# Kernel optimization log

Hardware: AMD Instinct MI355X
Metric: run time of the kernel (lower is better)

## Reference

```python
import jax, jax.numpy as jnp
import numpy as np

D_INV = 1024
N_HEADS = 8
D_HEAD = D_INV // N_HEADS
NEG_INF = -1e9  # masked-out logit value (adj_to_attn_mask)


def setup_inputs() -> dict:
    key = jax.random.key(0)
    ks = jax.random.split(key, 7)
    B, Nq, Nkv = 2, 2048, 2048
    v_inv = jax.random.normal(ks[0], (B, Nkv, D_INV), dtype=jnp.float32)
    messages = jax.random.normal(ks[1], (B, Nq, Nkv, N_HEADS), dtype=jnp.float32)
    adj_matrix = jax.random.randint(ks[2], (B, Nq, Nkv), 0, 2, dtype=jnp.int32)
    scale = 1.0 / np.sqrt(D_INV)
    in_w = jax.random.normal(ks[3], (D_INV, D_INV), dtype=jnp.float32) * scale
    in_b = jax.random.normal(ks[4], (D_INV,), dtype=jnp.float32) * 0.01
    out_w = jax.random.normal(ks[5], (D_INV, D_INV), dtype=jnp.float32) * scale
    out_b = jax.random.normal(ks[6], (D_INV,), dtype=jnp.float32) * 0.01
    return {"v_inv": v_inv, "messages": messages, "adj_matrix": adj_matrix,
            "in_w": in_w, "in_b": in_b, "out_w": out_w, "out_b": out_b}


def reference(v_inv, messages, adj_matrix, in_w, in_b, out_w, out_b):
    B, Nq, Nkv, H = messages.shape
    d_head = v_inv.shape[-1] // H
    # in_proj + split heads: [B, Nkv, H, d_head]
    proj = jnp.einsum('bkd,ed->bke', v_inv, in_w) + in_b
    head_feats = proj.reshape(B, Nkv, H, d_head)
    # adjacency -> additive mask, broadcast over heads
    attn_mask = jnp.where(adj_matrix != 0, 0.0, NEG_INF).astype(messages.dtype)
    logits = messages + attn_mask[..., None]            # [B, Nq, Nkv, H]
    attn = jax.nn.softmax(logits, axis=2)               # softmax over N_kv
    # per-head aggregation: [B, Nq, H, d_head]
    attn_out = jnp.einsum('bqkh,bkhd->bqhd', attn, head_feats)
    # L2-norm weight rescale over N_kv: [B, Nq, H]
    weights = jnp.sqrt(jnp.sum(attn * attn, axis=2))
    attn_out = attn_out * weights[..., None]
    attn_out = attn_out.reshape(B, Nq, H * d_head)
    return jnp.einsum('bqe,de->bqd', attn_out, out_w) + out_b
```

## Files before the change

kernel.cpp:

```cpp
#include <hip/hip_runtime.h>
#include <hip/hip_bf16.h>

typedef float f32x4 __attribute__((ext_vector_type(4)));
typedef __bf16 bf16x8 __attribute__((ext_vector_type(8)));

__device__ __forceinline__ unsigned short f2bf(float f) {
    union { float f; unsigned int u; } v; v.f = f;
    unsigned int u = v.u;
    unsigned int r = (u + 0x7fffu + ((u >> 16) & 1u)) >> 16;
    return (unsigned short)r;
}
__device__ __forceinline__ float bf2f(unsigned short u) {
    union { unsigned int u; float f; } v; v.u = ((unsigned int)u) << 16;
    return v.f;
}

__device__ __forceinline__ void block_sync_lgkm() {
    __asm__ __volatile__("" ::: "memory");
    __builtin_amdgcn_s_waitcnt(0xC07F);
    __builtin_amdgcn_s_barrier();
    __asm__ __volatile__("" ::: "memory");
}

__global__ __launch_bounds__(256) void k_cvt(const float* __restrict__ in,
                                             unsigned short* __restrict__ out, int n4) {
    int i = blockIdx.x * 256 + threadIdx.x;
    if (i >= n4) return;
    float4 v = ((const float4*)in)[i];
    ushort4 o;
    o.x = f2bf(v.x); o.y = f2bf(v.y); o.z = f2bf(v.z); o.w = f2bf(v.w);
    ((ushort4*)out)[i] = o;
}

__global__ __launch_bounds__(256, 4) void k_gemm_in(const unsigned short* __restrict__ A,
                                                    const unsigned short* __restrict__ B,
                                                    const float* __restrict__ bias,
                                                    unsigned short* __restrict__ Vfrag) {
    __shared__ __align__(16) unsigned short As[2][128 * 32];
    __shared__ __align__(16) unsigned short Bs[2][64 * 32];
    const int t = threadIdx.x;
    const int wv = t >> 6, lane = t & 63, mr = lane & 15, quad = lane >> 4;
    const int wi = wv >> 1, wj = wv & 1;
    const int m0 = blockIdx.y * 128, n0 = blockIdx.x * 64;

    f32x4 acc[4][2] = {};
    const int ra0 = t >> 2, ra1 = (t >> 2) + 64, rb = t >> 2;
    const int koff = (t & 3) * 8;

    uint4 pa0 = *(const uint4*)(A + (size_t)(m0 + ra0) * 1024 + koff);
    uint4 pa1 = *(const uint4*)(A + (size_t)(m0 + ra1) * 1024 + koff);
    uint4 pb  = *(const uint4*)(B + (size_t)(n0 + rb)  * 1024 + koff);

    for (int kb = 0; kb < 32; kb++) {
        unsigned short* as = As[kb & 1];
        unsigned short* bs = Bs[kb & 1];
        *(uint4*)&as[ra0 * 32 + koff] = pa0;
        *(uint4*)&as[ra1 * 32 + koff] = pa1;
        *(uint4*)&bs[rb  * 32 + koff] = pb;
        if (kb < 31) {
            int kk = (kb + 1) * 32 + koff;
            pa0 = *(const uint4*)(A + (size_t)(m0 + ra0) * 1024 + kk);
            pa1 = *(const uint4*)(A + (size_t)(m0 + ra1) * 1024 + kk);
            pb  = *(const uint4*)(B + (size_t)(n0 + rb)  * 1024 + kk);
        }
        block_sync_lgkm();
        bf16x8 af[4], bf[2];
        #pragma unroll
        for (int i = 0; i < 4; i++)
            af[i] = *(const bf16x8*)&as[(wi * 64 + i * 16 + mr) * 32 + quad * 8];
        #pragma unroll
        for (int j = 0; j < 2; j++)
            bf[j] = *(const bf16x8*)&bs[(wj * 32 + j * 16 + mr) * 32 + quad * 8];
        #pragma unroll
        for (int i = 0; i < 4; i++)
        #pragma unroll
        for (int j = 0; j < 2; j++)
            acc[i][j] = __builtin_amdgcn_mfma_f32_16x16x32_bf16(af[i], bf[j], acc[i][j], 0, 0, 0);
    }
    #pragma unroll
    for (int i = 0; i < 4; i++)
    #pragma unroll
    for (int j = 0; j < 2; j++) {
        int col = n0 + wj * 32 + j * 16 + mr;
        int row0 = m0 + wi * 64 + i * 16 + quad * 4;
        float be = bias[col];
        int h = col >> 7, d = col & 127;
        int bb = row0 >> 11, k = row0 & 2047;
        size_t idx8 = ((((size_t)(bb * 8 + h) * 64 + (k >> 5)) * 8 + (d >> 4)) * 64
                       + ((k >> 3) & 3) * 16 + (d & 15));
        int j0 = (quad & 1) * 4;
        ushort4 pk;
        pk.x = f2bf(acc[i][j][0] + be);
        pk.y = f2bf(acc[i][j][1] + be);
        pk.z = f2bf(acc[i][j][2] + be);
        pk.w = f2bf(acc[i][j][3] + be);
        *(ushort4*)(Vfrag + idx8 * 8 + j0) = pk;
    }
}

__global__ __launch_bounds__(256, 4) void k_gemm_out(const unsigned short* __restrict__ W,
                                                     const unsigned short* __restrict__ AOS,
                                                     const float* __restrict__ bias,
                                                     float* __restrict__ out) {
    __shared__ __align__(16) unsigned short As[2][128 * 32];
    __shared__ __align__(16) unsigned short Bs[2][64 * 32];
    const int t = threadIdx.x;
    const int wv = t >> 6, lane = t & 63, mr = lane & 15, quad = lane >> 4;
    const int wi = wv >> 1, wj = wv & 1;
    const int e0 = blockIdx.y * 128, r0 = blockIdx.x * 64;

    f32x4 acc[4][2] = {};
    const int ra0 = t >> 2, ra1 = (t >> 2) + 64, rb = t >> 2;
    const int koff = (t & 3) * 8;

    uint4 pa0 = *(const uint4*)(W   + (size_t)(e0 + ra0) * 1024 + koff);
    uint4 pa1 = *(const uint4*)(W   + (size_t)(e0 + ra1) * 1024 + koff);
    uint4 pb  = *(const uint4*)(AOS + (size_t)(r0 + rb)  * 1024 + koff);

    for (int kb = 0; kb < 32; kb++) {
        unsigned short* as = As[kb & 1];
        unsigned short* bs = Bs[kb & 1];
        *(uint4*)&as[ra0 * 32 + koff] = pa0;
        *(uint4*)&as[ra1 * 32 + koff] = pa1;
        *(uint4*)&bs[rb  * 32 + koff] = pb;
        if (kb < 31) {
            int kk = (kb + 1) * 32 + koff;
            pa0 = *(const uint4*)(W   + (size_t)(e0 + ra0) * 1024 + kk);
            pa1 = *(const uint4*)(W   + (size_t)(e0 + ra1) * 1024 + kk);
            pb  = *(const uint4*)(AOS + (size_t)(r0 + rb)  * 1024 + kk);
        }
        block_sync_lgkm();
        bf16x8 af[4], bf[2];
        #pragma unroll
        for (int i = 0; i < 4; i++)
            af[i] = *(const bf16x8*)&as[(wi * 64 + i * 16 + mr) * 32 + quad * 8];
        #pragma unroll
        for (int j = 0; j < 2; j++)
            bf[j] = *(const bf16x8*)&bs[(wj * 32 + j * 16 + mr) * 32 + quad * 8];
        #pragma unroll
        for (int i = 0; i < 4; i++)
        #pragma unroll
        for (int j = 0; j < 2; j++)
            acc[i][j] = __builtin_amdgcn_mfma_f32_16x16x32_bf16(af[i], bf[j], acc[i][j], 0, 0, 0);
    }
    #pragma unroll
    for (int i = 0; i < 4; i++)
    #pragma unroll
    for (int j = 0; j < 2; j++) {
        int r_ = r0 + wj * 32 + j * 16 + mr;
        int e_ = e0 + wi * 64 + i * 16 + quad * 4;
        float4 bv = *(const float4*)&bias[e_];
        float4 o;
        o.x = acc[i][j][0] + bv.x;
        o.y = acc[i][j][1] + bv.y;
        o.z = acc[i][j][2] + bv.z;
        o.w = acc[i][j][3] + bv.w;
        *(float4*)&out[(size_t)r_ * 1024 + e_] = o;
    }
}

__global__ __launch_bounds__(512, 2) void k_attn(const float* __restrict__ msg,
                                                 const int* __restrict__ adj,
                                                 const unsigned short* __restrict__ Vfrag,
                                                 unsigned short* __restrict__ AOS) {
    __shared__ __align__(16) unsigned short lds_p[2][4096];
    __shared__ float lds_w[8][16];
    __shared__ __align__(16) unsigned short lds_t[16 * 1032];

    const int t = threadIdx.x;
    const int wg = (int)blockIdx.x;
    const int swz = (wg & 7) * 32 + (wg >> 3);
    const int b = swz >> 7;
    const int q0 = (swz & 127) * 16;

    const int wv = t >> 6, lane = t & 63, mr = lane & 15, quad = lane >> 4;
    const int kl = lane >> 1;
    const int h0 = (lane & 1) * 4;
    const int lm0 = wv;

    const float* msg_base = msg + (size_t)(b * 2048 + q0) * 2048 * 8;
    const int* adj_base = adj + (size_t)(b * 2048 + q0) * 2048;
    const unsigned short* vf_base =
        Vfrag + (((size_t)(b * 8 + wv) * 64 * 8) * 64 + lane) * 8;

    const float* mp0 = msg_base + (size_t)lm0 * 16384 + kl * 8 + h0;
    const float* mp1 = mp0 + 8 * 16384;
    const int* ap0 = adj_base + lm0 * 2048 + kl;
    const int* ap1 = ap0 + 8 * 2048;

    float4 m0r = *(const float4*)mp0;
    float4 m1r = *(const float4*)mp1;
    int a0r = ap0[0], a1r = ap1[0];
    bf16x8 vfR[8];
    #pragma unroll
    for (int nc = 0; nc < 8; nc++) vfR[nc] = *(const bf16x8*)(vf_base + nc * 512);

    float laccs[2][4] = {}, saccs[2][4] = {};
    f32x4 acc[8] = {};

    const int sr = wv * 4 + quad;
    const int afrag_off = (sr * 16 + (mr ^ (sr & 15))) * 8;

    for (int kb = 0; kb < 64; kb++) {
        unsigned short* pbuf = lds_p[kb & 1];
        float px[2][4] = {{m0r.x, m0r.y, m0r.z, m0r.w}, {m1r.x, m1r.y, m1r.z, m1r.w}};
        float bl[2];
        bl[0] = a0r ? 0.f : -1e30f;
        bl[1] = a1r ? 0.f : -1e30f;
        #pragma unroll
        for (int qi = 0; qi < 2; qi++) {
            #pragma unroll
            for (int hj = 0; hj < 4; hj++) {
                float pe = __expf(px[qi][hj] + bl[qi]);
                laccs[qi][hj] += pe;
                saccs[qi][hj] = fmaf(pe, pe, saccs[qi][hj]);
                int s = (h0 + hj) * 4 + (kl >> 3);
                int m = lm0 + qi * 8;
                pbuf[(s * 16 + (m ^ (s & 15))) * 8 + (kl & 7)] = f2bf(pe);
            }
        }
        if (kb < 63) {
            m0r = *(const float4*)(mp0 + (kb + 1) * 256);
            m1r = *(const float4*)(mp1 + (kb + 1) * 256);
            a0r = ap0[(kb + 1) * 32];
            a1r = ap1[(kb + 1) * 32];
        }
        block_sync_lgkm();
        bf16x8 afrag = *(const bf16x8*)&pbuf[afrag_off];
        #pragma unroll
        for (int nc = 0; nc < 8; nc++)
            acc[nc] = __builtin_amdgcn_mfma_f32_16x16x32_bf16(afrag, vfR[nc], acc[nc], 0, 0, 0);
        if (kb < 63) {
            const unsigned short* vp = vf_base + (size_t)(kb + 1) * 4096;
            #pragma unroll
            for (int nc = 0; nc < 8; nc++) vfR[nc] = *(const bf16x8*)(vp + nc * 512);
        }
    }

    #pragma unroll
    for (int qi = 0; qi < 2; qi++)
    #pragma unroll
    for (int hj = 0; hj < 4; hj++) {
        float l = laccs[qi][hj], s = saccs[qi][hj];
        #pragma unroll
        for (int mdist = 2; mdist <= 32; mdist <<= 1) {
            l += __shfl_xor(l, mdist, 64);
            s += __shfl_xor(s, mdist, 64);
        }
        laccs[qi][hj] = l; saccs[qi][hj] = s;
    }
    if (lane < 2) {
        #pragma unroll
        for (int qi = 0; qi < 2; qi++)
        #pragma unroll
        for (int hj = 0; hj < 4; hj++) {
            float l = laccs[qi][hj];
            lds_w[lane * 4 + hj][wv + qi * 8] = __fsqrt_rn(saccs[qi][hj]) / (l * l);
        }
    }
    block_sync_lgkm();

    float4 wq = *(const float4*)&lds_w[wv][quad * 4];
    float wqa[4] = {wq.x, wq.y, wq.z, wq.w};
    #pragma unroll
    for (int nc = 0; nc < 8; nc++) {
        int e = wv * 128 + nc * 16 + mr;
        #pragma unroll
        for (int j = 0; j < 4; j++)
            lds_t[(quad * 4 + j) * 1032 + e] = f2bf(acc[nc][j] * wqa[j]);
    }
    block_sync_lgkm();
    #pragma unroll
    for (int p = 0; p < 4; p++) {
        int le = (p * 512 + t) * 8;
        int q = le >> 10, e = le & 1023;
        uint4 v = *(const uint4*)&lds_t[q * 1032 + e];
        *(uint4*)(AOS + (size_t)(b * 2048 + q0 + q) * 1024 + e) = v;
    }
}

extern "C" void kernel_launch(void* const* d_in, const int* in_sizes, int n_in,
                              void* d_out, int out_size, void* d_ws, size_t ws_size,
                              hipStream_t stream) {
    const float* v_inv    = (const float*)d_in[0];
    const float* messages = (const float*)d_in[1];
    const int*   adjm     = (const int*)d_in[2];
    const float* in_w     = (const float*)d_in[3];
    const float* in_b     = (const float*)d_in[4];
    const float* out_w    = (const float*)d_in[5];
    const float* out_b    = (const float*)d_in[6];
    float* out = (float*)d_out;

    char* ws = (char*)d_ws;
    unsigned short* vinv_bf = (unsigned short*)(ws);
    unsigned short* inw_bf  = (unsigned short*)(ws + (size_t)(8  << 20));
    unsigned short* outw_bf = (unsigned short*)(ws + (size_t)(10 << 20));
    unsigned short* Vfrag   = (unsigned short*)(ws + (size_t)(12 << 20));
    unsigned short* AOS     = (unsigned short*)(ws + (size_t)(20 << 20));

    hipLaunchKernelGGL(k_cvt, dim3(4096), dim3(256), 0, stream, v_inv, vinv_bf, 4194304 / 4);
    hipLaunchKernelGGL(k_cvt, dim3(1024), dim3(256), 0, stream, in_w, inw_bf, 1048576 / 4);
    hipLaunchKernelGGL(k_cvt, dim3(1024), dim3(256), 0, stream, out_w, outw_bf, 1048576 / 4);
    hipLaunchKernelGGL(k_gemm_in, dim3(16, 32), dim3(256), 0, stream, vinv_bf, inw_bf, in_b, Vfrag);
    hipLaunchKernelGGL(k_attn, dim3(256), dim3(512), 0, stream, messages, adjm, Vfrag, AOS);
    hipLaunchKernelGGL(k_gemm_out, dim3(64, 8), dim3(256), 0, stream, outw_bf, AOS, out_b, out);
}
```

Before: 460.9 us.

## Rework projection GEMMs with direct-to-LDS loads, triple buffering, larger tiles

Both projection GEMMs move to 128x128 tiles with a K step of 64. Tiles are staged straight into LDS with global_load_lds and a three-deep buffer ring managed by explicit vmcnt waits, replacing the register-staged double buffer. The three fp32-to-bf16 conversion launches are merged into one kernel to cut launch overhead. The larger LDS footprint (96 KB) and accumulator count lower occupancy, and the grids shrink to 256 blocks, which may underfill the device.

```diff
diff --git a/kernel.cpp b/kernel.cpp
--- a/kernel.cpp
+++ b/kernel.cpp
@@ -22,66 +22,92 @@
     __asm__ __volatile__("" ::: "memory");
 }
 
-__global__ __launch_bounds__(256) void k_cvt(const float* __restrict__ in,
-                                             unsigned short* __restrict__ out, int n4) {
-    int i = blockIdx.x * 256 + threadIdx.x;
-    if (i >= n4) return;
-    float4 v = ((const float4*)in)[i];
+__global__ __launch_bounds__(256) void k_cvt3(const float* __restrict__ a, unsigned short* __restrict__ oa,
+                                              const float* __restrict__ b, unsigned short* __restrict__ ob,
+                                              const float* __restrict__ c, unsigned short* __restrict__ oc) {
+    int id = blockIdx.x;
+    const float* src; unsigned short* dst; int i;
+    if (id < 4096)      { src = a; dst = oa; i = id * 256 + threadIdx.x; }
+    else if (id < 5120) { src = b; dst = ob; i = (id - 4096) * 256 + threadIdx.x; }
+    else                { src = c; dst = oc; i = (id - 5120) * 256 + threadIdx.x; }
+    float4 v = ((const float4*)src)[i];
     ushort4 o;
     o.x = f2bf(v.x); o.y = f2bf(v.y); o.z = f2bf(v.z); o.w = f2bf(v.w);
-    ((ushort4*)out)[i] = o;
-}
-
-__global__ __launch_bounds__(256, 4) void k_gemm_in(const unsigned short* __restrict__ A,
+    ((ushort4*)dst)[i] = o;
+}
+
+__device__ __forceinline__ void stage_tile(const unsigned short* __restrict__ g, int row0,
+                                           int ks, unsigned short* lds, int t) {
+    const int wv = t >> 6, lane = t & 63;
+    const unsigned short* gsrc = g + (size_t)(row0 + (lane >> 3)) * 1024 + ks * 64 + (lane & 7) * 8;
+    unsigned short* ldst = lds + wv * 512;
+    #pragma unroll
+    for (int i = 0; i < 4; i++) {
+        __builtin_amdgcn_global_load_lds(
+            (const __attribute__((address_space(1))) unsigned int*)(gsrc + (size_t)(i * 32 + wv * 8) * 1024),
+            (__attribute__((address_space(3))) unsigned int*)(ldst + i * 2048), 16, 0, 0);
+    }
+}
+
+__global__ __launch_bounds__(256, 2) void k_gemm_in(const unsigned short* __restrict__ A,
                                                     const unsigned short* __restrict__ B,
                                                     const float* __restrict__ bias,
                                                     unsigned short* __restrict__ Vfrag) {
-    __shared__ __align__(16) unsigned short As[2][128 * 32];
-    __shared__ __align__(16) unsigned short Bs[2][64 * 32];
+    __shared__ __align__(16) unsigned short As[3][128 * 64];
+    __shared__ __align__(16) unsigned short Bs[3][128 * 64];
     const int t = threadIdx.x;
     const int wv = t >> 6, lane = t & 63, mr = lane & 15, quad = lane >> 4;
     const int wi = wv >> 1, wj = wv & 1;
-    const int m0 = blockIdx.y * 128, n0 = blockIdx.x * 64;
-
-    f32x4 acc[4][2] = {};
-    const int ra0 = t >> 2, ra1 = (t >> 2) + 64, rb = t >> 2;
-    const int koff = (t & 3) * 8;
-
-    uint4 pa0 = *(const uint4*)(A + (size_t)(m0 + ra0) * 1024 + koff);
-    uint4 pa1 = *(const uint4*)(A + (size_t)(m0 + ra1) * 1024 + koff);
-    uint4 pb  = *(const uint4*)(B + (size_t)(n0 + rb)  * 1024 + koff);
-
-    for (int kb = 0; kb < 32; kb++) {
-        unsigned short* as = As[kb & 1];
-        unsigned short* bs = Bs[kb & 1];
-        *(uint4*)&as[ra0 * 32 + koff] = pa0;
-        *(uint4*)&as[ra1 * 32 + koff] = pa1;
-        *(uint4*)&bs[rb  * 32 + koff] = pb;
-        if (kb < 31) {
-            int kk = (kb + 1) * 32 + koff;
-            pa0 = *(const uint4*)(A + (size_t)(m0 + ra0) * 1024 + kk);
-            pa1 = *(const uint4*)(A + (size_t)(m0 + ra1) * 1024 + kk);
-            pb  = *(const uint4*)(B + (size_t)(n0 + rb)  * 1024 + kk);
-        }
+    const int m0 = blockIdx.y * 128, n0 = blockIdx.x * 128;
+
+    f32x4 acc[4][4] = {};
+
+    stage_tile(A, m0, 0, &As[0][0], t);
+    stage_tile(B, n0, 0, &Bs[0][0], t);
+    stage_tile(A, m0, 1, &As[1][0], t);
+    stage_tile(B, n0, 1, &Bs[1][0], t);
+
+    int cur = 0, nxt = 2;
+    for (int ks = 0; ks < 16; ks++) {
+        if (ks < 14) {
+            stage_tile(A, m0, ks + 2, &As[nxt][0], t);
+            stage_tile(B, n0, ks + 2, &Bs[nxt][0], t);
+            asm volatile("s_waitcnt vmcnt(16)" ::: "memory");
+        } else if (ks == 14) {
+            asm volatile("s_waitcnt vmcnt(8)" ::: "memory");
+        } else {
+            asm volatile("s_waitcnt vmcnt(0)" ::: "memory");
+        }
+        __builtin_amdgcn_s_barrier();
+        const unsigned short* as = &As[cur][0];
+        const unsigned short* bs = &Bs[cur][0];
+        bf16x8 af[2][4], bf[2][4];
+        #pragma unroll
+        for (int kk = 0; kk < 2; kk++) {
+            #pragma unroll
+            for (int i = 0; i < 4; i++)
+                af[kk][i] = *(const bf16x8*)&as[(wi * 64 + i * 16 + mr) * 64 + kk * 32 + quad * 8];
+            #pragma unroll
+            for (int j = 0; j < 4; j++)
+                bf[kk][j] = *(const bf16x8*)&bs[(wj * 64 + j * 16 + mr) * 64 + kk * 32 + quad * 8];
+        }
+        #pragma unroll
+        for (int kk = 0; kk < 2; kk++)
+        #pragma unroll
+        for (int i = 0; i < 4; i++)
+        #pragma unroll
+        for (int j = 0; j < 4; j++)
+            acc[i][j] = __builtin_amdgcn_mfma_f32_16x16x32_bf16(af[kk][i], bf[kk][j], acc[i][j], 0, 0, 0);
         block_sync_lgkm();
-        bf16x8 af[4], bf[2];
-        #pragma unroll
-        for (int i = 0; i < 4; i++)
-            af[i] = *(const bf16x8*)&as[(wi * 64 + i * 16 + mr) * 32 + quad * 8];
-        #pragma unroll
-        for (int j = 0; j < 2; j++)
-            bf[j] = *(const bf16x8*)&bs[(wj * 32 + j * 16 + mr) * 32 + quad * 8];
-        #pragma unroll
-        for (int i = 0; i < 4; i++)
-        #pragma unroll
-        for (int j = 0; j < 2; j++)
-            acc[i][j] = __builtin_amdgcn_mfma_f32_16x16x32_bf16(af[i], bf[j], acc[i][j], 0, 0, 0);
-    }
+        cur = cur == 2 ? 0 : cur + 1;
+        nxt = nxt == 2 ? 0 : nxt + 1;
+    }
+
     #pragma unroll
     for (int i = 0; i < 4; i++)
     #pragma unroll
-    for (int j = 0; j < 2; j++) {
-        int col = n0 + wj * 32 + j * 16 + mr;
+    for (int j = 0; j < 4; j++) {
+        int col = n0 + wj * 64 + j * 16 + mr;
         int row0 = m0 + wi * 64 + i * 16 + quad * 4;
         float be = bias[col];
         int h = col >> 7, d = col & 127;
@@ -98,56 +124,65 @@
     }
 }
 
-__global__ __launch_bounds__(256, 4) void k_gemm_out(const unsigned short* __restrict__ W,
+__global__ __launch_bounds__(256, 2) void k_gemm_out(const unsigned short* __restrict__ W,
                                                      const unsigned short* __restrict__ AOS,
                                                      const float* __restrict__ bias,
                                                      float* __restrict__ out) {
-    __shared__ __align__(16) unsigned short As[2][128 * 32];
-    __shared__ __align__(16) unsigned short Bs[2][64 * 32];
+    __shared__ __align__(16) unsigned short As[3][128 * 64];
+    __shared__ __align__(16) unsigned short Bs[3][128 * 64];
     const int t = threadIdx.x;
     const int wv = t >> 6, lane = t & 63, mr = lane & 15, quad = lane >> 4;
     const int wi = wv >> 1, wj = wv & 1;
-    const int e0 = blockIdx.y * 128, r0 = blockIdx.x * 64;
-
-    f32x4 acc[4][2] = {};
-    const int ra0 = t >> 2, ra1 = (t >> 2) + 64, rb = t >> 2;
-    const int koff = (t & 3) * 8;
-
-    uint4 pa0 = *(const uint4*)(W   + (size_t)(e0 + ra0) * 1024 + koff);
-    uint4 pa1 = *(const uint4*)(W   + (size_t)(e0 + ra1) * 1024 + koff);
-    uint4 pb  = *(const uint4*)(AOS + (size_t)(r0 + rb)  * 1024 + koff);
-
-    for (int kb = 0; kb < 32; kb++) {
-        unsigned short* as = As[kb & 1];
-        unsigned short* bs = Bs[kb & 1];
-        *(uint4*)&as[ra0 * 32 + koff] = pa0;
-        *(uint4*)&as[ra1 * 32 + koff] = pa1;
-        *(uint4*)&bs[rb  * 32 + koff] = pb;
-        if (kb < 31) {
-            int kk = (kb + 1) * 32 + koff;
-            pa0 = *(const uint4*)(W   + (size_t)(e0 + ra0) * 1024 + kk);
-            pa1 = *(const uint4*)(W   + (size_t)(e0 + ra1) * 1024 + kk);
-            pb  = *(const uint4*)(AOS + (size_t)(r0 + rb)  * 1024 + kk);
-        }
+    const int e0 = blockIdx.y * 128, r0 = blockIdx.x * 128;
+
+    f32x4 acc[4][4] = {};
+
+    stage_tile(W, e0, 0, &As[0][0], t);
+    stage_tile(AOS, r0, 0, &Bs[0][0], t);
+    stage_tile(W, e0, 1, &As[1][0], t);
+    stage_tile(AOS, r0, 1, &Bs[1][0], t);
+
+    int cur = 0, nxt = 2;
+    for (int ks = 0; ks < 16; ks++) {
+        if (ks < 14) {
+            stage_tile(W, e0, ks + 2, &As[nxt][0], t);
+            stage_tile(AOS, r0, ks + 2, &Bs[nxt][0], t);
+            asm volatile("s_waitcnt vmcnt(16)" ::: "memory");
+        } else if (ks == 14) {
+            asm volatile("s_waitcnt vmcnt(8)" ::: "memory");
+        } else {
+            asm volatile("s_waitcnt vmcnt(0)" ::: "memory");
+        }
+        __builtin_amdgcn_s_barrier();
+        const unsigned short* as = &As[cur][0];
+        const unsigned short* bs = &Bs[cur][0];
+        bf16x8 af[2][4], bf[2][4];
+        #pragma unroll
+        for (int kk = 0; kk < 2; kk++) {
+            #pragma unroll
+            for (int i = 0; i < 4; i++)
+                af[kk][i] = *(const bf16x8*)&as[(wi * 64 + i * 16 + mr) * 64 + kk * 32 + quad * 8];
+            #pragma unroll
+            for (int j = 0; j < 4; j++)
+                bf[kk][j] = *(const bf16x8*)&bs[(wj * 64 + j * 16 + mr) * 64 + kk * 32 + quad * 8];
+        }
+        #pragma unroll
+        for (int kk = 0; kk < 2; kk++)
+        #pragma unroll
+        for (int i = 0; i < 4; i++)
+        #pragma unroll
+        for (int j = 0; j < 4; j++)
+            acc[i][j] = __builtin_amdgcn_mfma_f32_16x16x32_bf16(af[kk][i], bf[kk][j], acc[i][j], 0, 0, 0);
         block_sync_lgkm();
-        bf16x8 af[4], bf[2];
-        #pragma unroll
-        for (int i = 0; i < 4; i++)
-            af[i] = *(const bf16x8*)&as[(wi * 64 + i * 16 + mr) * 32 + quad * 8];
-        #pragma unroll
-        for (int j = 0; j < 2; j++)
-            bf[j] = *(const bf16x8*)&bs[(wj * 32 + j * 16 + mr) * 32 + quad * 8];
-        #pragma unroll
-        for (int i = 0; i < 4; i++)
-        #pragma unroll
-        for (int j = 0; j < 2; j++)
-            acc[i][j] = __builtin_amdgcn_mfma_f32_16x16x32_bf16(af[i], bf[j], acc[i][j], 0, 0, 0);
-    }
+        cur = cur == 2 ? 0 : cur + 1;
+        nxt = nxt == 2 ? 0 : nxt + 1;
+    }
+
     #pragma unroll
     for (int i = 0; i < 4; i++)
     #pragma unroll
-    for (int j = 0; j < 2; j++) {
-        int r_ = r0 + wj * 32 + j * 16 + mr;
+    for (int j = 0; j < 4; j++) {
+        int r_ = r0 + wj * 64 + j * 16 + mr;
         int e_ = e0 + wi * 64 + i * 16 + quad * 4;
         float4 bv = *(const float4*)&bias[e_];
         float4 o;
@@ -298,10 +333,9 @@
     unsigned short* Vfrag   = (unsigned short*)(ws + (size_t)(12 << 20));
     unsigned short* AOS     = (unsigned short*)(ws + (size_t)(20 << 20));
 
-    hipLaunchKernelGGL(k_cvt, dim3(4096), dim3(256), 0, stream, v_inv, vinv_bf, 4194304 / 4);
-    hipLaunchKernelGGL(k_cvt, dim3(1024), dim3(256), 0, stream, in_w, inw_bf, 1048576 / 4);
-    hipLaunchKernelGGL(k_cvt, dim3(1024), dim3(256), 0, stream, out_w, outw_bf, 1048576 / 4);
-    hipLaunchKernelGGL(k_gemm_in, dim3(16, 32), dim3(256), 0, stream, vinv_bf, inw_bf, in_b, Vfrag);
+    hipLaunchKernelGGL(k_cvt3, dim3(6144), dim3(256), 0, stream,
+                       v_inv, vinv_bf, in_w, inw_bf, out_w, outw_bf);
+    hipLaunchKernelGGL(k_gemm_in, dim3(8, 32), dim3(256), 0, stream, vinv_bf, inw_bf, in_b, Vfrag);
     hipLaunchKernelGGL(k_attn, dim3(256), dim3(512), 0, stream, messages, adjm, Vfrag, AOS);
-    hipLaunchKernelGGL(k_gemm_out, dim3(64, 8), dim3(256), 0, stream, outw_bf, AOS, out_b, out);
-}
+    hipLaunchKernelGGL(k_gemm_out, dim3(32, 8), dim3(256), 0, stream, outw_bf, AOS, out_b, out);
+}
```

Result: slower. 472.2 us (+2.5%).

## Split attention workgroups by head half and fuse three conversion kernels

Applied to the files above, without the earlier changes.

The attention kernel now splits each 16-query tile across two workgroups of 256 threads, each handling four heads. This doubles the grid from 256 to 512 blocks and halves the per-block LDS, with the XCD swizzle adjusted to match. The three fp32-to-bf16 conversion launches are merged into one kernel to cut launch overhead. The split changes the message access pattern: each lane now reads a 4-float head half per key, so each block reads only half of every 32-byte message row.

```diff
diff --git a/kernel.cpp b/kernel.cpp
--- a/kernel.cpp
+++ b/kernel.cpp
@@ -22,14 +22,18 @@
     __asm__ __volatile__("" ::: "memory");
 }
 
-__global__ __launch_bounds__(256) void k_cvt(const float* __restrict__ in,
-                                             unsigned short* __restrict__ out, int n4) {
-    int i = blockIdx.x * 256 + threadIdx.x;
-    if (i >= n4) return;
-    float4 v = ((const float4*)in)[i];
+__global__ __launch_bounds__(256) void k_cvt3(const float* __restrict__ a, unsigned short* __restrict__ oa,
+                                              const float* __restrict__ b, unsigned short* __restrict__ ob,
+                                              const float* __restrict__ c, unsigned short* __restrict__ oc) {
+    int id = blockIdx.x;
+    const float* src; unsigned short* dst; int i;
+    if (id < 4096)      { src = a; dst = oa; i = id * 256 + threadIdx.x; }
+    else if (id < 5120) { src = b; dst = ob; i = (id - 4096) * 256 + threadIdx.x; }
+    else                { src = c; dst = oc; i = (id - 5120) * 256 + threadIdx.x; }
+    float4 v = ((const float4*)src)[i];
     ushort4 o;
     o.x = f2bf(v.x); o.y = f2bf(v.y); o.z = f2bf(v.z); o.w = f2bf(v.w);
-    ((ushort4*)out)[i] = o;
+    ((ushort4*)dst)[i] = o;
 }
 
 __global__ __launch_bounds__(256, 4) void k_gemm_in(const unsigned short* __restrict__ A,
@@ -159,33 +163,36 @@
     }
 }
 
-__global__ __launch_bounds__(512, 2) void k_attn(const float* __restrict__ msg,
+__global__ __launch_bounds__(256, 2) void k_attn(const float* __restrict__ msg,
                                                  const int* __restrict__ adj,
                                                  const unsigned short* __restrict__ Vfrag,
                                                  unsigned short* __restrict__ AOS) {
-    __shared__ __align__(16) unsigned short lds_p[2][4096];
-    __shared__ float lds_w[8][16];
-    __shared__ __align__(16) unsigned short lds_t[16 * 1032];
+    __shared__ __align__(16) unsigned short lds_p[2][2048];
+    __shared__ float lds_w[4][16];
+    __shared__ __align__(16) unsigned short lds_t[16 * 520];
 
     const int t = threadIdx.x;
     const int wg = (int)blockIdx.x;
-    const int swz = (wg & 7) * 32 + (wg >> 3);
-    const int b = swz >> 7;
-    const int q0 = (swz & 127) * 16;
+    const int xcd = wg & 7, idx = wg >> 3;
+    const int tile = xcd * 32 + (idx >> 1);
+    const int hb = idx & 1;
+    const int b = tile >> 7;
+    const int q0 = (tile & 127) * 16;
 
     const int wv = t >> 6, lane = t & 63, mr = lane & 15, quad = lane >> 4;
     const int kl = lane >> 1;
-    const int h0 = (lane & 1) * 4;
-    const int lm0 = wv;
+    const int par = lane & 1;
+    const int u = wv * 2 + par;
 
     const float* msg_base = msg + (size_t)(b * 2048 + q0) * 2048 * 8;
     const int* adj_base = adj + (size_t)(b * 2048 + q0) * 2048;
+    const int gh = hb * 4 + wv;
     const unsigned short* vf_base =
-        Vfrag + (((size_t)(b * 8 + wv) * 64 * 8) * 64 + lane) * 8;
-
-    const float* mp0 = msg_base + (size_t)lm0 * 16384 + kl * 8 + h0;
+        Vfrag + (((size_t)(b * 8 + gh) * 64 * 8) * 64 + lane) * 8;
+
+    const float* mp0 = msg_base + (size_t)u * 16384 + kl * 8 + hb * 4;
     const float* mp1 = mp0 + 8 * 16384;
-    const int* ap0 = adj_base + lm0 * 2048 + kl;
+    const int* ap0 = adj_base + u * 2048 + kl;
     const int* ap1 = ap0 + 8 * 2048;
 
     float4 m0r = *(const float4*)mp0;
@@ -210,12 +217,12 @@
         #pragma unroll
         for (int qi = 0; qi < 2; qi++) {
             #pragma unroll
-            for (int hj = 0; hj < 4; hj++) {
-                float pe = __expf(px[qi][hj] + bl[qi]);
-                laccs[qi][hj] += pe;
-                saccs[qi][hj] = fmaf(pe, pe, saccs[qi][hj]);
-                int s = (h0 + hj) * 4 + (kl >> 3);
-                int m = lm0 + qi * 8;
+            for (int hl = 0; hl < 4; hl++) {
+                float pe = __expf(px[qi][hl] + bl[qi]);
+                laccs[qi][hl] += pe;
+                saccs[qi][hl] = fmaf(pe, pe, saccs[qi][hl]);
+                int s = hl * 4 + (kl >> 3);
+                int m = u + qi * 8;
                 pbuf[(s * 16 + (m ^ (s & 15))) * 8 + (kl & 7)] = f2bf(pe);
             }
         }
@@ -240,22 +247,22 @@
     #pragma unroll
     for (int qi = 0; qi < 2; qi++)
     #pragma unroll
-    for (int hj = 0; hj < 4; hj++) {
-        float l = laccs[qi][hj], s = saccs[qi][hj];
+    for (int hl = 0; hl < 4; hl++) {
+        float l = laccs[qi][hl], s = saccs[qi][hl];
         #pragma unroll
         for (int mdist = 2; mdist <= 32; mdist <<= 1) {
             l += __shfl_xor(l, mdist, 64);
             s += __shfl_xor(s, mdist, 64);
         }
-        laccs[qi][hj] = l; saccs[qi][hj] = s;
+        laccs[qi][hl] = l; saccs[qi][hl] = s;
     }
     if (lane < 2) {
         #pragma unroll
         for (int qi = 0; qi < 2; qi++)
         #pragma unroll
-        for (int hj = 0; hj < 4; hj++) {
-            float l = laccs[qi][hj];
-            lds_w[lane * 4 + hj][wv + qi * 8] = __fsqrt_rn(saccs[qi][hj]) / (l * l);
+        for (int hl = 0; hl < 4; hl++) {
+            float l = laccs[qi][hl];
+            lds_w[hl][wv * 2 + lane + qi * 8] = __fsqrt_rn(saccs[qi][hl]) / (l * l);
         }
     }
     block_sync_lgkm();
@@ -267,15 +274,15 @@
         int e = wv * 128 + nc * 16 + mr;
         #pragma unroll
         for (int j = 0; j < 4; j++)
-            lds_t[(quad * 4 + j) * 1032 + e] = f2bf(acc[nc][j] * wqa[j]);
+            lds_t[(quad * 4 + j) * 520 + e] = f2bf(acc[nc][j] * wqa[j]);
     }
     block_sync_lgkm();
     #pragma unroll
     for (int p = 0; p < 4; p++) {
-        int le = (p * 512 + t) * 8;
-        int q = le >> 10, e = le & 1023;
-        uint4 v = *(const uint4*)&lds_t[q * 1032 + e];
-        *(uint4*)(AOS + (size_t)(b * 2048 + q0 + q) * 1024 + e) = v;
+        int le = (p * 256 + t) * 8;
+        int q = le >> 9, e = le & 511;
+        uint4 v = *(const uint4*)&lds_t[q * 520 + e];
+        *(uint4*)(AOS + (size_t)(b * 2048 + q0 + q) * 1024 + hb * 512 + e) = v;
     }
 }
 
@@ -298,10 +305,9 @@
     unsigned short* Vfrag   = (unsigned short*)(ws + (size_t)(12 << 20));
     unsigned short* AOS     = (unsigned short*)(ws + (size_t)(20 << 20));
 
-    hipLaunchKernelGGL(k_cvt, dim3(4096), dim3(256), 0, stream, v_inv, vinv_bf, 4194304 / 4);
-    hipLaunchKernelGGL(k_cvt, dim3(1024), dim3(256), 0, stream, in_w, inw_bf, 1048576 / 4);
-    hipLaunchKernelGGL(k_cvt, dim3(1024), dim3(256), 0, stream, out_w, outw_bf, 1048576 / 4);
+    hipLaunchKernelGGL(k_cvt3, dim3(6144), dim3(256), 0, stream,
+                       v_inv, vinv_bf, in_w, inw_bf, out_w, outw_bf);
     hipLaunchKernelGGL(k_gemm_in, dim3(16, 32), dim3(256), 0, stream, vinv_bf, inw_bf, in_b, Vfrag);
-    hipLaunchKernelGGL(k_attn, dim3(256), dim3(512), 0, stream, messages, adjm, Vfrag, AOS);
+    hipLaunchKernelGGL(k_attn, dim3(512), dim3(256), 0, stream, messages, adjm, Vfrag, AOS);
     hipLaunchKernelGGL(k_gemm_out, dim3(64, 8), dim3(256), 0, stream, outw_bf, AOS, out_b, out);
 }
```

Result: no change. 462.5 us (+0.3%).

## Use direct global-to-LDS loads in GEMMs and fuse bf16 conversion launches

Applied to the files above, without the earlier changes.

Both projection GEMMs now stage tiles with global_load_lds, which writes global data straight into shared memory instead of going through registers, and use a single wait-plus-barrier per k-step with double buffering. The three fp32-to-bf16 conversion launches are merged into one kernel that picks its source by block index. This removes register staging, LDS write instructions and two kernel launches. The risk is that waiting on vmcnt(0) each iteration limits overlap, and the wave-level LDS write layout must match the existing fragment-read layout.

```diff
diff --git a/kernel.cpp b/kernel.cpp
--- a/kernel.cpp
+++ b/kernel.cpp
@@ -22,14 +22,35 @@
     __asm__ __volatile__("" ::: "memory");
 }
 
-__global__ __launch_bounds__(256) void k_cvt(const float* __restrict__ in,
-                                             unsigned short* __restrict__ out, int n4) {
-    int i = blockIdx.x * 256 + threadIdx.x;
-    if (i >= n4) return;
-    float4 v = ((const float4*)in)[i];
+__global__ __launch_bounds__(256) void k_cvt3(const float* __restrict__ a, unsigned short* __restrict__ oa,
+                                              const float* __restrict__ b, unsigned short* __restrict__ ob,
+                                              const float* __restrict__ c, unsigned short* __restrict__ oc) {
+    int id = blockIdx.x;
+    const float* src; unsigned short* dst; int i;
+    if (id < 4096)      { src = a; dst = oa; i = id * 256 + threadIdx.x; }
+    else if (id < 5120) { src = b; dst = ob; i = (id - 4096) * 256 + threadIdx.x; }
+    else                { src = c; dst = oc; i = (id - 5120) * 256 + threadIdx.x; }
+    float4 v = ((const float4*)src)[i];
     ushort4 o;
     o.x = f2bf(v.x); o.y = f2bf(v.y); o.z = f2bf(v.z); o.w = f2bf(v.w);
-    ((ushort4*)out)[i] = o;
+    ((ushort4*)dst)[i] = o;
+}
+
+__device__ __forceinline__ void stage2(const unsigned short* __restrict__ gA, int rowA,
+                                       const unsigned short* __restrict__ gB, int rowB,
+                                       int k0, unsigned short* as, unsigned short* bs,
+                                       int wv, int lane) {
+    const unsigned short* sa = gA + (size_t)(rowA + wv * 16 + (lane >> 2)) * 1024 + k0 + (lane & 3) * 8;
+    const unsigned short* sb = gB + (size_t)(rowB + wv * 16 + (lane >> 2)) * 1024 + k0 + (lane & 3) * 8;
+    __builtin_amdgcn_global_load_lds(
+        (const __attribute__((address_space(1))) unsigned int*)sa,
+        (__attribute__((address_space(3))) unsigned int*)(as + wv * 512), 16, 0, 0);
+    __builtin_amdgcn_global_load_lds(
+        (const __attribute__((address_space(1))) unsigned int*)(sa + (size_t)64 * 1024),
+        (__attribute__((address_space(3))) unsigned int*)(as + 2048 + wv * 512), 16, 0, 0);
+    __builtin_amdgcn_global_load_lds(
+        (const __attribute__((address_space(1))) unsigned int*)sb,
+        (__attribute__((address_space(3))) unsigned int*)(bs + wv * 512), 16, 0, 0);
 }
 
 __global__ __launch_bounds__(256, 4) void k_gemm_in(const unsigned short* __restrict__ A,
@@ -44,26 +65,17 @@
     const int m0 = blockIdx.y * 128, n0 = blockIdx.x * 64;
 
     f32x4 acc[4][2] = {};
-    const int ra0 = t >> 2, ra1 = (t >> 2) + 64, rb = t >> 2;
-    const int koff = (t & 3) * 8;
-
-    uint4 pa0 = *(const uint4*)(A + (size_t)(m0 + ra0) * 1024 + koff);
-    uint4 pa1 = *(const uint4*)(A + (size_t)(m0 + ra1) * 1024 + koff);
-    uint4 pb  = *(const uint4*)(B + (size_t)(n0 + rb)  * 1024 + koff);
-
+
+    stage2(A, m0, B, n0, 0, As[0], Bs[0], wv, lane);
+    asm volatile("s_waitcnt vmcnt(0)" ::: "memory");
+    __builtin_amdgcn_s_barrier();
+
+    int cur = 0;
     for (int kb = 0; kb < 32; kb++) {
-        unsigned short* as = As[kb & 1];
-        unsigned short* bs = Bs[kb & 1];
-        *(uint4*)&as[ra0 * 32 + koff] = pa0;
-        *(uint4*)&as[ra1 * 32 + koff] = pa1;
-        *(uint4*)&bs[rb  * 32 + koff] = pb;
-        if (kb < 31) {
-            int kk = (kb + 1) * 32 + koff;
-            pa0 = *(const uint4*)(A + (size_t)(m0 + ra0) * 1024 + kk);
-            pa1 = *(const uint4*)(A + (size_t)(m0 + ra1) * 1024 + kk);
-            pb  = *(const uint4*)(B + (size_t)(n0 + rb)  * 1024 + kk);
-        }
-        block_sync_lgkm();
+        if (kb < 31)
+            stage2(A, m0, B, n0, (kb + 1) * 32, As[cur ^ 1], Bs[cur ^ 1], wv, lane);
+        const unsigned short* as = As[cur];
+        const unsigned short* bs = Bs[cur];
         bf16x8 af[4], bf[2];
         #pragma unroll
         for (int i = 0; i < 4; i++)
@@ -76,6 +88,9 @@
         #pragma unroll
         for (int j = 0; j < 2; j++)
             acc[i][j] = __builtin_amdgcn_mfma_f32_16x16x32_bf16(af[i], bf[j], acc[i][j], 0, 0, 0);
+        asm volatile("s_waitcnt vmcnt(0)" ::: "memory");
+        __builtin_amdgcn_s_barrier();
+        cur ^= 1;
     }
     #pragma unroll
     for (int i = 0; i < 4; i++)
@@ -110,26 +125,17 @@
     const int e0 = blockIdx.y * 128, r0 = blockIdx.x * 64;
 
     f32x4 acc[4][2] = {};
-    const int ra0 = t >> 2, ra1 = (t >> 2) + 64, rb = t >> 2;
-    const int koff = (t & 3) * 8;
-
-    uint4 pa0 = *(const uint4*)(W   + (size_t)(e0 + ra0) * 1024 + koff);
-    uint4 pa1 = *(const uint4*)(W   + (size_t)(e0 + ra1) * 1024 + koff);
-    uint4 pb  = *(const uint4*)(AOS + (size_t)(r0 + rb)  * 1024 + koff);
-
+
+    stage2(W, e0, AOS, r0, 0, As[0], Bs[0], wv, lane);
+    asm volatile("s_waitcnt vmcnt(0)" ::: "memory");
+    __builtin_amdgcn_s_barrier();
+
+    int cur = 0;
     for (int kb = 0; kb < 32; kb++) {
-        unsigned short* as = As[kb & 1];
-        unsigned short* bs = Bs[kb & 1];
-        *(uint4*)&as[ra0 * 32 + koff] = pa0;
-        *(uint4*)&as[ra1 * 32 + koff] = pa1;
-        *(uint4*)&bs[rb  * 32 + koff] = pb;
-        if (kb < 31) {
-            int kk = (kb + 1) * 32 + koff;
-            pa0 = *(const uint4*)(W   + (size_t)(e0 + ra0) * 1024 + kk);
-            pa1 = *(const uint4*)(W   + (size_t)(e0 + ra1) * 1024 + kk);
-            pb  = *(const uint4*)(AOS + (size_t)(r0 + rb)  * 1024 + kk);
-        }
-        block_sync_lgkm();
+        if (kb < 31)
+            stage2(W, e0, AOS, r0, (kb + 1) * 32, As[cur ^ 1], Bs[cur ^ 1], wv, lane);
+        const unsigned short* as = As[cur];
+        const unsigned short* bs = Bs[cur];
         bf16x8 af[4], bf[2];
         #pragma unroll
         for (int i = 0; i < 4; i++)
@@ -142,6 +148,9 @@
         #pragma unroll
         for (int j = 0; j < 2; j++)
             acc[i][j] = __builtin_amdgcn_mfma_f32_16x16x32_bf16(af[i], bf[j], acc[i][j], 0, 0, 0);
+        asm volatile("s_waitcnt vmcnt(0)" ::: "memory");
+        __builtin_amdgcn_s_barrier();
+        cur ^= 1;
     }
     #pragma unroll
     for (int i = 0; i < 4; i++)
@@ -298,9 +307,8 @@
     unsigned short* Vfrag   = (unsigned short*)(ws + (size_t)(12 << 20));
     unsigned short* AOS     = (unsigned short*)(ws + (size_t)(20 << 20));
 
-    hipLaunchKernelGGL(k_cvt, dim3(4096), dim3(256), 0, stream, v_inv, vinv_bf, 4194304 / 4);
-    hipLaunchKernelGGL(k_cvt, dim3(1024), dim3(256), 0, stream, in_w, inw_bf, 1048576 / 4);
-    hipLaunchKernelGGL(k_cvt, dim3(1024), dim3(256), 0, stream, out_w, outw_bf, 1048576 / 4);
+    hipLaunchKernelGGL(k_cvt3, dim3(6144), dim3(256), 0, stream,
+                       v_inv, vinv_bf, in_w, inw_bf, out_w, outw_bf);
     hipLaunchKernelGGL(k_gemm_in, dim3(16, 32), dim3(256), 0, stream, vinv_bf, inw_bf, in_b, Vfrag);
     hipLaunchKernelGGL(k_attn, dim3(256), dim3(512), 0, stream, messages, adjm, Vfrag, AOS);
     hipLaunchKernelGGL(k_gemm_out, dim3(64, 8), dim3(256), 0, stream, outw_bf, AOS, out_b, out);
```

Result: no change. 465.0 us (+0.9%).
